# Performance work log

Hardware: AMD Instinct MI355X
Metric: run time of the kernel (lower is better)

The kernel has to match this reference:

```python
import jax, jax.numpy as jnp
import numpy as np

HID = 512      # hidden_dim
SEQ = 784      # sequence length hard-coded via make_discrete_HiPPO_nojit(hidden, 784)
BATCH = 1024
OUT = 10


def make_discrete_hippo(N, L):
    # HiPPO-LegS continuous matrices (standard construction)
    n = np.arange(N, dtype=np.float64)
    P = np.sqrt(1.0 + 2.0 * n)
    A = P[:, None] * P[None, :]
    A = -(np.tril(A) - np.diag(n))          # (N, N)
    B = np.sqrt(2.0 * n + 1.0).reshape(N, 1)  # (N, 1)
    # bilinear (Tustin) discretization with step = 1/L
    step = 1.0 / L
    I = np.eye(N)
    BL = np.linalg.inv(I - (step / 2.0) * A)
    Ad = BL @ (I + (step / 2.0) * A)
    Bd = (BL * step) @ B
    return jnp.asarray(Ad, jnp.float32), jnp.asarray(Bd[:, 0], jnp.float32)


def setup_inputs() -> dict:
    key = jax.random.key(0)
    k1, k2, k3, k4 = jax.random.split(key, 4)
    x = jax.random.normal(k1, (BATCH, SEQ), jnp.float32)
    # xavier-uniform C params (flax nn.initializers.xavier_uniform)
    a0 = float(np.sqrt(6.0 / (1 + HID)))
    a1 = float(np.sqrt(6.0 / (HID + HID)))
    C0 = jax.random.uniform(k2, (1, HID), jnp.float32, -a0, a0)
    C1 = jax.random.uniform(k3, (HID, HID), jnp.float32, -a1, a1)
    # final Dense(output_dim): lecun_normal kernel, zero bias
    W = jax.random.normal(k4, (HID, OUT), jnp.float32) / np.sqrt(HID)
    b = jnp.zeros((OUT,), jnp.float32)
    return {"x": x, "C0": C0, "C1": C1, "W": W, "b": b}


def _ssm_layer(A, Bvec, C, u):
    # u: (batch, seq) scalar input per step; returns ys: (seq, batch, d_out)
    def step(h, u_t):  # h: (batch, HID), u_t: (batch,)
        h_next = jnp.tanh(h @ A.T + u_t[:, None] * Bvec[None, :])
        y = h_next @ C.T
        return h_next, y
    h0 = jnp.zeros((u.shape[0], HID), u.dtype)
    _, ys = jax.lax.scan(step, h0, u.T)
    return ys


def reference(x, C0, C1, W, b):
    A, Bvec = make_discrete_hippo(HID, SEQ)  # trace-time constants
    y0 = _ssm_layer(A, Bvec, C0, x)[:, :, 0].T   # (batch, seq) scalar stream
    y1 = _ssm_layer(A, Bvec, C1, y0)             # (seq, batch, HID)
    logits = y1[-1] @ W + b                      # last timestep -> Dense
    return logits
```

## Files before the change

kernel.cpp:

```cpp
#include <hip/hip_runtime.h>
#include <math.h>

#define SEQL 784
#define HIDN 512
#define OUTD 10

typedef float v2 __attribute__((ext_vector_type(2)));

template<int CTRL, int RM>
__device__ __forceinline__ float dpp0(float v) {
    int r = __builtin_amdgcn_update_dpp(0, __builtin_bit_cast(int, v),
                                        CTRL, RM, 0xF, true);
    return __builtin_bit_cast(float, r);
}
__device__ __forceinline__ v2 sp(float v) { v2 r; r.x = v; r.y = v; return r; }
__device__ __forceinline__ v2 vfma(v2 a, v2 b, v2 c) {
    return __builtin_elementwise_fma(a, b, c);
}

__global__ __launch_bounds__(256) void compute_M(const float* __restrict__ C1,
                                                 const float* __restrict__ W,
                                                 float* __restrict__ M) {
    __shared__ float Ws[HIDN * OUTD];
    __shared__ float red[4][64][OUTD];
    const int lane = threadIdx.x & 63, w = threadIdx.x >> 6;
    const int i = blockIdx.x * 64 + lane;
    for (int idx = threadIdx.x; idx < HIDN * OUTD; idx += 256) Ws[idx] = W[idx];
    __syncthreads();
    float acc[OUTD];
#pragma unroll
    for (int o = 0; o < OUTD; ++o) acc[o] = 0.f;
    for (int j = w * 128; j < w * 128 + 128; ++j) {
        float cv = C1[j * HIDN + i];
#pragma unroll
        for (int o = 0; o < OUTD; ++o) acc[o] = fmaf(cv, Ws[j * OUTD + o], acc[o]);
    }
#pragma unroll
    for (int o = 0; o < OUTD; ++o) red[w][lane][o] = acc[o];
    __syncthreads();
    if (w == 0) {
#pragma unroll
        for (int o = 0; o < OUTD; ++o)
            M[i * OUTD + o] = (red[0][lane][o] + red[1][lane][o]) +
                              (red[2][lane][o] + red[3][lane][o]);
    }
}

__global__ __launch_bounds__(256, 1) void ssm_main(const float* __restrict__ x,
                                                   const float* __restrict__ C0,
                                                   const float* __restrict__ Mmat,
                                                   const float* __restrict__ bias,
                                                   float* __restrict__ out) {
    const int tid = threadIdx.x;
    const int wave = tid >> 6;
    const int lane = tid & 63;
    const int row = blockIdx.x * 4 + wave;

    __shared__ float xs[4][SEQL + 2];
    __shared__ float Ms[HIDN * OUTD];

    const float DEL = 1.0f / 784.0f;
    for (int idx = tid; idx < 4 * SEQL; idx += 256)
        xs[idx / SEQL][idx % SEQL] = DEL * x[blockIdx.x * 4 * SEQL + idx];
    if (tid < 8) xs[tid >> 1][SEQL + (tid & 1)] = 0.f;
    __syncthreads();

    const double cd = 1.0 / 1568.0;
    const double F = 2.0 * 1.4426950408889634;
    float P[8], Ps[8], a_[8], G2[8], mE2[8], K1[8], K2[8], Bd2[8], C0d[8];
    double apD = 0.0, bpD = 1.0;
    double aL = 1.0, bL = 0.0;
#pragma unroll
    for (int j = 0; j < 8; ++j) {
        int i = lane * 8 + j;
        double Pd = sqrt(1.0 + 2.0 * (double)i);
        double dd = 1.0 + cd * (double)(i + 1);
        double fd = 1.0 / dd;
        double ad = (1.0 - cd * (double)i) * fd;
        double mEd = -cd * Pd * fd;
        double ed = Pd * mEd;
        double Gd = (1.0 - cd * (double)(i + 1)) * fd;
        K2[j] = (float)(F * mEd * (1.0 + apD));
        K1[j] = (float)(F * mEd * bpD);
        apD = ad * apD + ed;
        bpD = ad * bpD;
        P[j]   = (float)Pd;
        Ps[j]  = (float)(Pd / F);
        a_[j]  = (float)ad;
        G2[j]  = (float)(F * Gd);
        mE2[j] = (float)(F * mEd);
        C0d[j] = DEL * C0[i];
        bL = ad * bL + Pd * Pd * fd;
        aL *= ad;
    }
    float ac[6], bc[6];
    {
        double al = apD, be = bpD;
        int rl = lane & 15;
#pragma unroll
        for (int L = 0; L < 4; ++L) {
            int d = 1 << L;
            ac[L] = (float)al; bc[L] = (float)be;
            double pa = __shfl_up(al, d, 64);
            double pb = __shfl_up(be, d, 64);
            if (rl >= d) { al += be * pa; be *= pb; }
        }
        ac[4] = (float)al; bc[4] = (float)be;
        {
            int src = (lane & 32) + 15;
            double pa = __shfl(al, src, 64);
            double pb = __shfl(be, src, 64);
            if (lane & 16) { al += be * pa; be *= pb; }
        }
        ac[5] = (float)al; bc[5] = (float)be;
        {
            double pa = __shfl(al, 31, 64);
            double pb = __shfl(be, 31, 64);
            if (lane >= 32) { al += be * pa; be *= pb; }
        }
    }
    {
        double A = aL, B = bL;
#pragma unroll
        for (int d = 1; d < 64; d <<= 1) {
            double pA = __shfl_up(A, d, 64);
            double pB = __shfl_up(B, d, 64);
            if (lane >= d) { B = A * pB + B; A *= pA; }
        }
        double sIn = __shfl_up(B, 1, 64);
        double s = lane ? sIn : 0.0;
#pragma unroll
        for (int j = 0; j < 8; ++j) {
            int i = lane * 8 + j;
            double Pd = sqrt(1.0 + 2.0 * (double)i);
            double fd = 1.0 / (1.0 + cd * (double)(i + 1));
            double ad = (1.0 - cd * (double)i) * fd;
            Bd2[j] = (float)(F * (Pd - cd * Pd * s) * fd);
            s = ad * s + Pd * Pd * fd;
        }
    }

    v2 h[8];
#pragma unroll
    for (int j = 0; j < 8; ++j) h[j] = sp(0.f);

    float y0s = 0.f;
    float u1 = xs[wave][0];

#pragma unroll 2
    for (int k = 0; k < SEQL + 1; ++k) {
        float u_next = xs[wave][k + 1];
        v2 du; du.x = u1; du.y = y0s;

        v2 inner[8], sb[8];
        v2 r = sp(0.f), s = sp(0.f);
#pragma unroll
        for (int j = 0; j < 8; ++j) {
            v2 hj = h[j];
            v2 in_ = vfma(sp(mE2[j]), r, sp(G2[j]) * hj);
            inner[j] = in_;
            sb[j] = s;
            s = vfma(sp(a_[j]), s, sp(Ps[j]) * in_);
            r = vfma(sp(P[j]), hj, r);
        }

#define LVL(CTRL, RM, L) {                                                   \
        s.x = fmaf(bc[L], dpp0<CTRL, RM>(s.x),                               \
                   fmaf(ac[L], dpp0<CTRL, RM>(r.x), s.x));                   \
        s.y = fmaf(bc[L], dpp0<CTRL, RM>(s.y),                               \
                   fmaf(ac[L], dpp0<CTRL, RM>(r.y), s.y));                   \
        r.x += dpp0<CTRL, RM>(r.x);                                          \
        r.y += dpp0<CTRL, RM>(r.y); }
        LVL(0x111, 0xF, 0)
        LVL(0x112, 0xF, 1)
        LVL(0x114, 0xF, 2)
        LVL(0x118, 0xF, 3)
        LVL(0x142, 0xA, 4)
        LVL(0x143, 0xC, 5)
#undef LVL
        v2 ri, si;
        ri.x = dpp0<0x138, 0xF>(r.x);  ri.y = dpp0<0x138, 0xF>(r.y);
        si.x = dpp0<0x138, 0xF>(s.x);  si.y = dpp0<0x138, 0xF>(s.y);

        float part = 0.f;
#pragma unroll
        for (int j = 0; j < 8; ++j) {
            v2 yy = vfma(sp(mE2[j]), sb[j], inner[j]);
            yy = vfma(sp(K2[j]), ri, yy);
            yy = vfma(sp(K1[j]), si, yy);
            yy = vfma(sp(Bd2[j]), du, yy);
            v2 e;  e.x = __builtin_amdgcn_exp2f(yy.x);
                   e.y = __builtin_amdgcn_exp2f(yy.y);
            v2 e1 = e + sp(1.f);
            v2 rc; rc.x = __builtin_amdgcn_rcpf(e1.x);
                   rc.y = __builtin_amdgcn_rcpf(e1.y);
            v2 hn = vfma(sp(-2.f), rc, sp(1.f));
            h[j] = hn;
            part = fmaf(C0d[j], hn.x, part);
        }
        part += dpp0<0x111, 0xF>(part);
        part += dpp0<0x112, 0xF>(part);
        part += dpp0<0x114, 0xF>(part);
        part += dpp0<0x118, 0xF>(part);
        part += dpp0<0x142, 0xA>(part);
        part += dpp0<0x143, 0xC>(part);
        y0s = __builtin_bit_cast(float,
                __builtin_amdgcn_readlane(__builtin_bit_cast(int, part), 63));
        u1 = u_next;
    }

    __syncthreads();
    for (int idx = tid; idx < HIDN * OUTD; idx += 256) Ms[idx] = Mmat[idx];
    __syncthreads();

    float acc[OUTD];
#pragma unroll
    for (int o = 0; o < OUTD; ++o) acc[o] = 0.f;
#pragma unroll
    for (int j = 0; j < 8; ++j) {
        float hv = h[j].y;
        int i = lane * 8 + j;
#pragma unroll
        for (int o = 0; o < OUTD; ++o) acc[o] = fmaf(hv, Ms[i * OUTD + o], acc[o]);
    }
#pragma unroll
    for (int o = 0; o < OUTD; ++o) {
#pragma unroll
        for (int d = 32; d; d >>= 1) acc[o] += __shfl_xor(acc[o], d, 64);
    }
    if (lane == 0) {
#pragma unroll
        for (int o = 0; o < OUTD; ++o) out[row * OUTD + o] = acc[o] + bias[o];
    }
}

extern "C" void kernel_launch(void* const* d_in, const int* in_sizes, int n_in,
                              void* d_out, int out_size, void* d_ws, size_t ws_size,
                              hipStream_t stream) {
    const float* x  = (const float*)d_in[0];
    const float* C0 = (const float*)d_in[1];
    const float* C1 = (const float*)d_in[2];
    const float* W  = (const float*)d_in[3];
    const float* b  = (const float*)d_in[4];
    float* M = (float*)d_ws;

    compute_M<<<dim3(8), dim3(256), 0, stream>>>(C1, W, M);
    ssm_main<<<dim3(256), dim3(256), 0, stream>>>(x, C0, M, b, (float*)d_out);
}
```

Measured before the change: 430.0 us.

## Split each batch row's hidden state across two waves with cross-wave scan carry

Each batch row's 512-element hidden state is now split over two waves of 256 elements each, so every lane holds 4 states instead of 8. The grid doubles to 512 blocks and launch bounds allow 2 blocks per CU. The carry of the lower half's prefix scan (r, s) is passed to the upper half through shared memory, and the y0 partial sums are combined there as well, with a double-buffered exchange. The aim is to shorten the per-step serial chain and use more of the machine, at the cost of a block-wide __syncthreads on every one of the 785 timesteps.

Result: slower. 591.3 us (+37.5%).

```diff
diff --git a/kernel.cpp b/kernel.cpp
--- a/kernel.cpp
+++ b/kernel.cpp
@@ -46,7 +46,7 @@
     }
 }
 
-__global__ __launch_bounds__(256, 1) void ssm_main(const float* __restrict__ x,
+__global__ __launch_bounds__(256, 2) void ssm_main(const float* __restrict__ x,
                                                    const float* __restrict__ C0,
                                                    const float* __restrict__ Mmat,
                                                    const float* __restrict__ bias,
@@ -54,25 +54,32 @@
     const int tid = threadIdx.x;
     const int wave = tid >> 6;
     const int lane = tid & 63;
-    const int row = blockIdx.x * 4 + wave;
-
-    __shared__ float xs[4][SEQL + 2];
+    const int rowl = wave >> 1;
+    const int half = wave & 1;
+    const int row = blockIdx.x * 2 + rowl;
+
+    __shared__ float xs[2][SEQL + 2];
+    __shared__ float tot[2][2][2][4];
+    __shared__ float y0p[2][2][2];
+    __shared__ double bdB[2];
+    __shared__ float red[2][2][OUTD];
     __shared__ float Ms[HIDN * OUTD];
 
     const float DEL = 1.0f / 784.0f;
-    for (int idx = tid; idx < 4 * SEQL; idx += 256)
-        xs[idx / SEQL][idx % SEQL] = DEL * x[blockIdx.x * 4 * SEQL + idx];
-    if (tid < 8) xs[tid >> 1][SEQL + (tid & 1)] = 0.f;
-    __syncthreads();
+    for (int idx = tid; idx < 2 * SEQL; idx += 256)
+        xs[idx / SEQL][idx % SEQL] = DEL * x[blockIdx.x * 2 * SEQL + idx];
+    if (tid < 4) xs[tid >> 1][SEQL + (tid & 1)] = 0.f;
+    if (tid < 32) ((float*)tot)[tid] = 0.f;
+    if (tid < 8) ((float*)y0p)[tid] = 0.f;
 
     const double cd = 1.0 / 1568.0;
     const double F = 2.0 * 1.4426950408889634;
-    float P[8], Ps[8], a_[8], G2[8], mE2[8], K1[8], K2[8], Bd2[8], C0d[8];
+    float P[4], Ps[4], a_[4], G2[4], mE2[4], K1[4], K2[4], Bd2[4], C0d[4];
     double apD = 0.0, bpD = 1.0;
     double aL = 1.0, bL = 0.0;
 #pragma unroll
-    for (int j = 0; j < 8; ++j) {
-        int i = lane * 8 + j;
+    for (int j = 0; j < 4; ++j) {
+        int i = half * 256 + lane * 4 + j;
         double Pd = sqrt(1.0 + 2.0 * (double)i);
         double dd = 1.0 + cd * (double)(i + 1);
         double fd = 1.0 / dd;
@@ -119,6 +126,20 @@
             if (lane >= 32) { al += be * pa; be *= pb; }
         }
     }
+    float Ain, Bin;
+    {
+        double A = apD, Bq = bpD;
+#pragma unroll
+        for (int d = 1; d < 64; d <<= 1) {
+            double pa = __shfl_up(A, d, 64);
+            double pb = __shfl_up(Bq, d, 64);
+            if (lane >= d) { A = Bq * pa + A; Bq *= pb; }
+        }
+        double Ae = __shfl_up(A, 1, 64);
+        double Be = __shfl_up(Bq, 1, 64);
+        if (lane == 0) { Ae = 0.0; Be = 1.0; }
+        Ain = (float)Ae; Bin = (float)Be;
+    }
     {
         double A = aL, B = bL;
 #pragma unroll
@@ -127,11 +148,16 @@
             double pB = __shfl_up(B, d, 64);
             if (lane >= d) { B = A * pB + B; A *= pA; }
         }
-        double sIn = __shfl_up(B, 1, 64);
-        double s = lane ? sIn : 0.0;
-#pragma unroll
-        for (int j = 0; j < 8; ++j) {
-            int i = lane * 8 + j;
+        double Aex = __shfl_up(A, 1, 64);
+        double Bex = __shfl_up(B, 1, 64);
+        if (lane == 0) { Aex = 1.0; Bex = 0.0; }
+        if (half == 0 && lane == 63) bdB[rowl] = B;
+        __syncthreads();
+        double sIn = half ? bdB[rowl] : 0.0;
+        double s = Aex * sIn + Bex;
+#pragma unroll
+        for (int j = 0; j < 4; ++j) {
+            int i = half * 256 + lane * 4 + j;
             double Pd = sqrt(1.0 + 2.0 * (double)i);
             double fd = 1.0 / (1.0 + cd * (double)(i + 1));
             double ad = (1.0 - cd * (double)i) * fd;
@@ -140,22 +166,20 @@
         }
     }
 
-    v2 h[8];
-#pragma unroll
-    for (int j = 0; j < 8; ++j) h[j] = sp(0.f);
-
-    float y0s = 0.f;
-    float u1 = xs[wave][0];
-
-#pragma unroll 2
+    v2 h[4];
+#pragma unroll
+    for (int j = 0; j < 4; ++j) h[j] = sp(0.f);
+
+    float u1 = xs[rowl][0];
+
     for (int k = 0; k < SEQL + 1; ++k) {
-        float u_next = xs[wave][k + 1];
-        v2 du; du.x = u1; du.y = y0s;
-
-        v2 inner[8], sb[8];
+        const int p = k & 1, q = p ^ 1;
+        float u_next = xs[rowl][k + 1];
+
+        v2 inner[4], sb[4];
         v2 r = sp(0.f), s = sp(0.f);
 #pragma unroll
-        for (int j = 0; j < 8; ++j) {
+        for (int j = 0; j < 4; ++j) {
             v2 hj = h[j];
             v2 in_ = vfma(sp(mE2[j]), r, sp(G2[j]) * hj);
             inner[j] = in_;
@@ -182,12 +206,26 @@
         ri.x = dpp0<0x138, 0xF>(r.x);  ri.y = dpp0<0x138, 0xF>(r.y);
         si.x = dpp0<0x138, 0xF>(s.x);  si.y = dpp0<0x138, 0xF>(s.y);
 
+        if (half == 0 && lane == 63) {
+            tot[p][rowl][1][0] = r.x; tot[p][rowl][1][1] = r.y;
+            tot[p][rowl][1][2] = s.x; tot[p][rowl][1][3] = s.y;
+        }
+        __syncthreads();
+
+        v2 rT, sT;
+        rT.x = tot[p][rowl][half][0]; rT.y = tot[p][rowl][half][1];
+        sT.x = tot[p][rowl][half][2]; sT.y = tot[p][rowl][half][3];
+        float y0s = y0p[q][rowl][0] + y0p[q][rowl][1];
+        v2 du; du.x = u1; du.y = y0s;
+        v2 rig = ri + rT;
+        v2 sig = vfma(sp(Bin), sT, vfma(sp(Ain), rT, si));
+
         float part = 0.f;
 #pragma unroll
-        for (int j = 0; j < 8; ++j) {
+        for (int j = 0; j < 4; ++j) {
             v2 yy = vfma(sp(mE2[j]), sb[j], inner[j]);
-            yy = vfma(sp(K2[j]), ri, yy);
-            yy = vfma(sp(K1[j]), si, yy);
+            yy = vfma(sp(K2[j]), rig, yy);
+            yy = vfma(sp(K1[j]), sig, yy);
             yy = vfma(sp(Bd2[j]), du, yy);
             v2 e;  e.x = __builtin_amdgcn_exp2f(yy.x);
                    e.y = __builtin_amdgcn_exp2f(yy.y);
@@ -204,8 +242,7 @@
         part += dpp0<0x118, 0xF>(part);
         part += dpp0<0x142, 0xA>(part);
         part += dpp0<0x143, 0xC>(part);
-        y0s = __builtin_bit_cast(float,
-                __builtin_amdgcn_readlane(__builtin_bit_cast(int, part), 63));
+        if (lane == 63) y0p[p][rowl][half] = part;
         u1 = u_next;
     }
 
@@ -217,9 +254,9 @@
 #pragma unroll
     for (int o = 0; o < OUTD; ++o) acc[o] = 0.f;
 #pragma unroll
-    for (int j = 0; j < 8; ++j) {
+    for (int j = 0; j < 4; ++j) {
         float hv = h[j].y;
-        int i = lane * 8 + j;
+        int i = half * 256 + lane * 4 + j;
 #pragma unroll
         for (int o = 0; o < OUTD; ++o) acc[o] = fmaf(hv, Ms[i * OUTD + o], acc[o]);
     }
@@ -230,7 +267,13 @@
     }
     if (lane == 0) {
 #pragma unroll
-        for (int o = 0; o < OUTD; ++o) out[row * OUTD + o] = acc[o] + bias[o];
+        for (int o = 0; o < OUTD; ++o) red[rowl][half][o] = acc[o];
+    }
+    __syncthreads();
+    if (half == 0 && lane == 0) {
+#pragma unroll
+        for (int o = 0; o < OUTD; ++o)
+            out[row * OUTD + o] = red[rowl][0][o] + red[rowl][1][o] + bias[o];
     }
 }
 
@@ -245,5 +288,5 @@
     float* M = (float*)d_ws;
 
     compute_M<<<dim3(8), dim3(256), 0, stream>>>(C1, W, M);
-    ssm_main<<<dim3(256), dim3(256), 0, stream>>>(x, C0, M, b, (float*)d_out);
-}
+    ssm_main<<<dim3(512), dim3(256), 0, stream>>>(x, C0, M, b, (float*)d_out);
+}
```

## Split the two SSM layers across two waves per batch row with LDS handoff

Applied to the files above, without the earlier changes.

Previously one wave per batch row ran both SSM layers in lockstep using packed 2-wide vector math. Now each block handles one row with two waves: wave 0 runs layer 0 and writes its scalar output into a double-buffered LDS slot, and wave 1 consumes it one step later for layer 1. This doubles the number of waves (1024 blocks of 128 threads) to fill more of the GPU and shortens each wave's dependency chain. In exchange it adds a block-wide barrier on every timestep and drops the packed FMA math. The final projection now reads M from global memory instead of staging it in LDS.

New measurement: 567.5 us. 32.0% more time.

```diff
diff --git a/kernel.cpp b/kernel.cpp
--- a/kernel.cpp
+++ b/kernel.cpp
@@ -4,18 +4,12 @@
 #define SEQL 784
 #define HIDN 512
 #define OUTD 10
-
-typedef float v2 __attribute__((ext_vector_type(2)));
 
 template<int CTRL, int RM>
 __device__ __forceinline__ float dpp0(float v) {
     int r = __builtin_amdgcn_update_dpp(0, __builtin_bit_cast(int, v),
                                         CTRL, RM, 0xF, true);
     return __builtin_bit_cast(float, r);
-}
-__device__ __forceinline__ v2 sp(float v) { v2 r; r.x = v; r.y = v; return r; }
-__device__ __forceinline__ v2 vfma(v2 a, v2 b, v2 c) {
-    return __builtin_elementwise_fma(a, b, c);
 }
 
 __global__ __launch_bounds__(256) void compute_M(const float* __restrict__ C1,
@@ -46,7 +40,7 @@
     }
 }
 
-__global__ __launch_bounds__(256, 1) void ssm_main(const float* __restrict__ x,
+__global__ __launch_bounds__(128, 2) void ssm_main(const float* __restrict__ x,
                                                    const float* __restrict__ C0,
                                                    const float* __restrict__ Mmat,
                                                    const float* __restrict__ bias,
@@ -54,16 +48,15 @@
     const int tid = threadIdx.x;
     const int wave = tid >> 6;
     const int lane = tid & 63;
-    const int row = blockIdx.x * 4 + wave;
-
-    __shared__ float xs[4][SEQL + 2];
-    __shared__ float Ms[HIDN * OUTD];
+    const int row = blockIdx.x;
+
+    __shared__ float xs[SEQL + 2];
+    __shared__ float y0buf[2];
 
     const float DEL = 1.0f / 784.0f;
-    for (int idx = tid; idx < 4 * SEQL; idx += 256)
-        xs[idx / SEQL][idx % SEQL] = DEL * x[blockIdx.x * 4 * SEQL + idx];
-    if (tid < 8) xs[tid >> 1][SEQL + (tid & 1)] = 0.f;
-    __syncthreads();
+    for (int idx = tid; idx < SEQL; idx += 128)
+        xs[idx] = DEL * x[row * SEQL + idx];
+    if (tid < 2) { xs[SEQL + tid] = 0.f; y0buf[tid] = 0.f; }
 
     const double cd = 1.0 / 1568.0;
     const double F = 2.0 * 1.4426950408889634;
@@ -139,38 +132,37 @@
             s = ad * s + Pd * Pd * fd;
         }
     }
-
-    v2 h[8];
-#pragma unroll
-    for (int j = 0; j < 8; ++j) h[j] = sp(0.f);
-
-    float y0s = 0.f;
-    float u1 = xs[wave][0];
+    __syncthreads();
+
+    float h[8];
+#pragma unroll
+    for (int j = 0; j < 8; ++j) h[j] = 0.f;
+
+    float u1 = xs[0];
 
 #pragma unroll 2
     for (int k = 0; k < SEQL + 1; ++k) {
-        float u_next = xs[wave][k + 1];
-        v2 du; du.x = u1; du.y = y0s;
-
-        v2 inner[8], sb[8];
-        v2 r = sp(0.f), s = sp(0.f);
-#pragma unroll
-        for (int j = 0; j < 8; ++j) {
-            v2 hj = h[j];
-            v2 in_ = vfma(sp(mE2[j]), r, sp(G2[j]) * hj);
+        const int p = k & 1, q = p ^ 1;
+        float yprev = y0buf[q];
+        float du = wave ? yprev : u1;
+        float u_next = xs[k + 1];
+
+        float inner[8], sb[8];
+        float r = 0.f, s = 0.f;
+#pragma unroll
+        for (int j = 0; j < 8; ++j) {
+            float hj = h[j];
+            float in_ = fmaf(mE2[j], r, G2[j] * hj);
             inner[j] = in_;
             sb[j] = s;
-            s = vfma(sp(a_[j]), s, sp(Ps[j]) * in_);
-            r = vfma(sp(P[j]), hj, r);
+            s = fmaf(a_[j], s, Ps[j] * in_);
+            r = fmaf(P[j], hj, r);
         }
 
 #define LVL(CTRL, RM, L) {                                                   \
-        s.x = fmaf(bc[L], dpp0<CTRL, RM>(s.x),                               \
-                   fmaf(ac[L], dpp0<CTRL, RM>(r.x), s.x));                   \
-        s.y = fmaf(bc[L], dpp0<CTRL, RM>(s.y),                               \
-                   fmaf(ac[L], dpp0<CTRL, RM>(r.y), s.y));                   \
-        r.x += dpp0<CTRL, RM>(r.x);                                          \
-        r.y += dpp0<CTRL, RM>(r.y); }
+        s = fmaf(bc[L], dpp0<CTRL, RM>(s),                                   \
+                 fmaf(ac[L], dpp0<CTRL, RM>(r), s));                         \
+        r += dpp0<CTRL, RM>(r); }
         LVL(0x111, 0xF, 0)
         LVL(0x112, 0xF, 1)
         LVL(0x114, 0xF, 2)
@@ -178,59 +170,56 @@
         LVL(0x142, 0xA, 4)
         LVL(0x143, 0xC, 5)
 #undef LVL
-        v2 ri, si;
-        ri.x = dpp0<0x138, 0xF>(r.x);  ri.y = dpp0<0x138, 0xF>(r.y);
-        si.x = dpp0<0x138, 0xF>(s.x);  si.y = dpp0<0x138, 0xF>(s.y);
+        float ri = dpp0<0x138, 0xF>(r);
+        float si = dpp0<0x138, 0xF>(s);
 
         float part = 0.f;
 #pragma unroll
         for (int j = 0; j < 8; ++j) {
-            v2 yy = vfma(sp(mE2[j]), sb[j], inner[j]);
-            yy = vfma(sp(K2[j]), ri, yy);
-            yy = vfma(sp(K1[j]), si, yy);
-            yy = vfma(sp(Bd2[j]), du, yy);
-            v2 e;  e.x = __builtin_amdgcn_exp2f(yy.x);
-                   e.y = __builtin_amdgcn_exp2f(yy.y);
-            v2 e1 = e + sp(1.f);
-            v2 rc; rc.x = __builtin_amdgcn_rcpf(e1.x);
-                   rc.y = __builtin_amdgcn_rcpf(e1.y);
-            v2 hn = vfma(sp(-2.f), rc, sp(1.f));
+            float yy = fmaf(mE2[j], sb[j], inner[j]);
+            yy = fmaf(K2[j], ri, yy);
+            yy = fmaf(K1[j], si, yy);
+            yy = fmaf(Bd2[j], du, yy);
+            float e = __builtin_amdgcn_exp2f(yy);
+            float rc = __builtin_amdgcn_rcpf(e + 1.f);
+            float hn = fmaf(-2.f, rc, 1.f);
             h[j] = hn;
-            part = fmaf(C0d[j], hn.x, part);
-        }
-        part += dpp0<0x111, 0xF>(part);
-        part += dpp0<0x112, 0xF>(part);
-        part += dpp0<0x114, 0xF>(part);
-        part += dpp0<0x118, 0xF>(part);
-        part += dpp0<0x142, 0xA>(part);
-        part += dpp0<0x143, 0xC>(part);
-        y0s = __builtin_bit_cast(float,
-                __builtin_amdgcn_readlane(__builtin_bit_cast(int, part), 63));
+            part = fmaf(C0d[j], hn, part);
+        }
+        if (wave == 0) {
+            part += dpp0<0x111, 0xF>(part);
+            part += dpp0<0x112, 0xF>(part);
+            part += dpp0<0x114, 0xF>(part);
+            part += dpp0<0x118, 0xF>(part);
+            part += dpp0<0x142, 0xA>(part);
+            part += dpp0<0x143, 0xC>(part);
+            if (lane == 63) y0buf[p] = part;
+        }
+        __syncthreads();
         u1 = u_next;
     }
 
-    __syncthreads();
-    for (int idx = tid; idx < HIDN * OUTD; idx += 256) Ms[idx] = Mmat[idx];
-    __syncthreads();
-
-    float acc[OUTD];
-#pragma unroll
-    for (int o = 0; o < OUTD; ++o) acc[o] = 0.f;
-#pragma unroll
-    for (int j = 0; j < 8; ++j) {
-        float hv = h[j].y;
-        int i = lane * 8 + j;
-#pragma unroll
-        for (int o = 0; o < OUTD; ++o) acc[o] = fmaf(hv, Ms[i * OUTD + o], acc[o]);
-    }
-#pragma unroll
-    for (int o = 0; o < OUTD; ++o) {
-#pragma unroll
-        for (int d = 32; d; d >>= 1) acc[o] += __shfl_xor(acc[o], d, 64);
-    }
-    if (lane == 0) {
-#pragma unroll
-        for (int o = 0; o < OUTD; ++o) out[row * OUTD + o] = acc[o] + bias[o];
+    if (wave == 1) {
+        float acc[OUTD];
+#pragma unroll
+        for (int o = 0; o < OUTD; ++o) acc[o] = 0.f;
+#pragma unroll
+        for (int j = 0; j < 8; ++j) {
+            float hv = h[j];
+            int i = lane * 8 + j;
+#pragma unroll
+            for (int o = 0; o < OUTD; ++o)
+                acc[o] = fmaf(hv, Mmat[i * OUTD + o], acc[o]);
+        }
+#pragma unroll
+        for (int o = 0; o < OUTD; ++o) {
+#pragma unroll
+            for (int d = 32; d; d >>= 1) acc[o] += __shfl_xor(acc[o], d, 64);
+        }
+        if (lane == 0) {
+#pragma unroll
+            for (int o = 0; o < OUTD; ++o) out[row * OUTD + o] = acc[o] + bias[o];
+        }
     }
 }
 
@@ -245,5 +234,5 @@
     float* M = (float*)d_ws;
 
     compute_M<<<dim3(8), dim3(256), 0, stream>>>(C1, W, M);
-    ssm_main<<<dim3(256), dim3(256), 0, stream>>>(x, C0, M, b, (float*)d_out);
-}
+    ssm_main<<<dim3(1024), dim3(128), 0, stream>>>(x, C0, M, b, (float*)d_out);
+}
```

## Fold input term into recurrence and delay y0 stream to simplify per-step math

Applied to the files above, without the earlier changes.

Folds the Bd*u input contribution into the inner term before the in-lane scan, so the output pass runs a running S recurrence instead of four separate FMAs with K1/K2/Bd2 coefficients. This removes the double-precision Bd2 prefix-scan setup. The layer-1 input now uses y0 delayed by two steps, and the loop runs one extra iteration to match. It also drops the LDS staging of M and reads it straight from global memory in the epilogue. The per-step FMA count falls, but the serial dependency through S in the output loop grows, and rounding changes.

Result: slower. 443.2 us (+3.1%).

```diff
diff --git a/kernel.cpp b/kernel.cpp
--- a/kernel.cpp
+++ b/kernel.cpp
@@ -56,20 +56,18 @@
     const int lane = tid & 63;
     const int row = blockIdx.x * 4 + wave;
 
-    __shared__ float xs[4][SEQL + 2];
-    __shared__ float Ms[HIDN * OUTD];
+    __shared__ float xs[4][SEQL + 3];
 
     const float DEL = 1.0f / 784.0f;
     for (int idx = tid; idx < 4 * SEQL; idx += 256)
         xs[idx / SEQL][idx % SEQL] = DEL * x[blockIdx.x * 4 * SEQL + idx];
-    if (tid < 8) xs[tid >> 1][SEQL + (tid & 1)] = 0.f;
+    if (tid < 12) xs[tid / 3][SEQL + (tid % 3)] = 0.f;
     __syncthreads();
 
     const double cd = 1.0 / 1568.0;
     const double F = 2.0 * 1.4426950408889634;
-    float P[8], Ps[8], a_[8], G2[8], mE2[8], K1[8], K2[8], Bd2[8], C0d[8];
+    float P[8], Ps[8], a_[8], G2[8], mE2[8], FT[8], C0d[8];
     double apD = 0.0, bpD = 1.0;
-    double aL = 1.0, bL = 0.0;
 #pragma unroll
     for (int j = 0; j < 8; ++j) {
         int i = lane * 8 + j;
@@ -80,8 +78,6 @@
         double mEd = -cd * Pd * fd;
         double ed = Pd * mEd;
         double Gd = (1.0 - cd * (double)(i + 1)) * fd;
-        K2[j] = (float)(F * mEd * (1.0 + apD));
-        K1[j] = (float)(F * mEd * bpD);
         apD = ad * apD + ed;
         bpD = ad * bpD;
         P[j]   = (float)Pd;
@@ -89,9 +85,8 @@
         a_[j]  = (float)ad;
         G2[j]  = (float)(F * Gd);
         mE2[j] = (float)(F * mEd);
+        FT[j]  = (float)(F * Pd * fd);
         C0d[j] = DEL * C0[i];
-        bL = ad * bL + Pd * Pd * fd;
-        aL *= ad;
     }
     float ac[6], bc[6];
     {
@@ -119,48 +114,30 @@
             if (lane >= 32) { al += be * pa; be *= pb; }
         }
     }
-    {
-        double A = aL, B = bL;
-#pragma unroll
-        for (int d = 1; d < 64; d <<= 1) {
-            double pA = __shfl_up(A, d, 64);
-            double pB = __shfl_up(B, d, 64);
-            if (lane >= d) { B = A * pB + B; A *= pA; }
-        }
-        double sIn = __shfl_up(B, 1, 64);
-        double s = lane ? sIn : 0.0;
-#pragma unroll
-        for (int j = 0; j < 8; ++j) {
-            int i = lane * 8 + j;
-            double Pd = sqrt(1.0 + 2.0 * (double)i);
-            double fd = 1.0 / (1.0 + cd * (double)(i + 1));
-            double ad = (1.0 - cd * (double)i) * fd;
-            Bd2[j] = (float)(F * (Pd - cd * Pd * s) * fd);
-            s = ad * s + Pd * Pd * fd;
-        }
-    }
 
     v2 h[8];
 #pragma unroll
     for (int j = 0; j < 8; ++j) h[j] = sp(0.f);
 
-    float y0s = 0.f;
+    float y0_d1 = 0.f, y0_d2 = 0.f;
     float u1 = xs[wave][0];
 
 #pragma unroll 2
-    for (int k = 0; k < SEQL + 1; ++k) {
+    for (int k = 0; k < SEQL + 2; ++k) {
         float u_next = xs[wave][k + 1];
-        v2 du; du.x = u1; du.y = y0s;
-
-        v2 inner[8], sb[8];
+        v2 du; du.x = u1; du.y = y0_d2;
+
+        v2 inn[8], zz[8];
         v2 r = sp(0.f), s = sp(0.f);
 #pragma unroll
         for (int j = 0; j < 8; ++j) {
             v2 hj = h[j];
             v2 in_ = vfma(sp(mE2[j]), r, sp(G2[j]) * hj);
-            inner[j] = in_;
-            sb[j] = s;
-            s = vfma(sp(a_[j]), s, sp(Ps[j]) * in_);
+            in_ = vfma(sp(FT[j]), du, in_);
+            inn[j] = in_;
+            v2 z = sp(Ps[j]) * in_;
+            zz[j] = z;
+            s = vfma(sp(a_[j]), s, z);
             r = vfma(sp(P[j]), hj, r);
         }
 
@@ -182,13 +159,12 @@
         ri.x = dpp0<0x138, 0xF>(r.x);  ri.y = dpp0<0x138, 0xF>(r.y);
         si.x = dpp0<0x138, 0xF>(s.x);  si.y = dpp0<0x138, 0xF>(s.y);
 
+        v2 S = ri + si;
         float part = 0.f;
 #pragma unroll
         for (int j = 0; j < 8; ++j) {
-            v2 yy = vfma(sp(mE2[j]), sb[j], inner[j]);
-            yy = vfma(sp(K2[j]), ri, yy);
-            yy = vfma(sp(K1[j]), si, yy);
-            yy = vfma(sp(Bd2[j]), du, yy);
+            v2 yy = vfma(sp(mE2[j]), S, inn[j]);
+            S = vfma(sp(a_[j]), S, zz[j]);
             v2 e;  e.x = __builtin_amdgcn_exp2f(yy.x);
                    e.y = __builtin_amdgcn_exp2f(yy.y);
             v2 e1 = e + sp(1.f);
@@ -204,14 +180,11 @@
         part += dpp0<0x118, 0xF>(part);
         part += dpp0<0x142, 0xA>(part);
         part += dpp0<0x143, 0xC>(part);
-        y0s = __builtin_bit_cast(float,
-                __builtin_amdgcn_readlane(__builtin_bit_cast(int, part), 63));
+        y0_d2 = y0_d1;
+        y0_d1 = __builtin_bit_cast(float,
+                  __builtin_amdgcn_readlane(__builtin_bit_cast(int, part), 63));
         u1 = u_next;
     }
-
-    __syncthreads();
-    for (int idx = tid; idx < HIDN * OUTD; idx += 256) Ms[idx] = Mmat[idx];
-    __syncthreads();
 
     float acc[OUTD];
 #pragma unroll
@@ -221,7 +194,8 @@
         float hv = h[j].y;
         int i = lane * 8 + j;
 #pragma unroll
-        for (int o = 0; o < OUTD; ++o) acc[o] = fmaf(hv, Ms[i * OUTD + o], acc[o]);
+        for (int o = 0; o < OUTD; ++o)
+            acc[o] = fmaf(hv, Mmat[i * OUTD + o], acc[o]);
     }
 #pragma unroll
     for (int o = 0; o < OUTD; ++o) {
```
